# Optimization experiments

Hardware: AMD Instinct MI355X
Metric: run time of the kernel (lower is better)

## Reference

```python
import jax, jax.numpy as jnp
import numpy as np

BN_EPS = 1e-5


def _feat_proj(x, w1, w2, gamma, beta):
    # FactorLinear2D: (N,L,C) @ w2^T -> (N,L,K); weighted sum over L with w1^T -> (N,K)
    h = jnp.einsum('nlc,kc->nlk', x, w2)
    h = jnp.einsum('nlk,kl->nk', h, w1)
    # BatchNorm1d, training mode (biased batch stats), affine
    mu = h.mean(axis=0)
    var = h.var(axis=0)
    return gamma * (h - mu) * jax.lax.rsqrt(var + BN_EPS) + beta


def setup_inputs() -> dict:
    key = jax.random.key(0)
    ks = jax.random.split(key, 16)
    N, G, H, P, K = 64, 8, 1024, 2048, 39548
    s = 0.02
    return {
        'x0': jax.random.normal(ks[0], (N, 257, 1024), jnp.float32),
        'x1': jax.random.normal(ks[1], (N, 197, 768), jnp.float32),
        'w1_0': s * jax.random.normal(ks[2], (H, 257), jnp.float32),
        'w2_0': s * jax.random.normal(ks[3], (H, 1024), jnp.float32),
        'gamma0': jnp.ones((H,), jnp.float32),
        'beta0': jnp.zeros((H,), jnp.float32),
        'w1_1': s * jax.random.normal(ks[4], (H, 197), jnp.float32),
        'w2_1': s * jax.random.normal(ks[5], (H, 768), jnp.float32),
        'gamma1': jnp.ones((H,), jnp.float32),
        'beta1': jnp.zeros((H,), jnp.float32),
        'shared_w': s * jax.random.normal(ks[6], (P, H), jnp.float32),
        'fc_w': s * jax.random.normal(ks[7], (G * P, H), jnp.float32),
        'fc_b': s * jax.random.normal(ks[8], (G * P,), jnp.float32),
        'embed_w': s * jax.random.normal(ks[9], (K, P), jnp.float32),
        'embed_b': s * jax.random.normal(ks[10], (K,), jnp.float32),
        'indices': jax.random.randint(ks[11], (64,), 0, G, jnp.int64),
    }


def reference(x0, x1, w1_0, w2_0, gamma0, beta0, w1_1, w2_1, gamma1, beta1,
              shared_w, fc_w, fc_b, embed_w, embed_b, indices):
    G = 8
    h0 = _feat_proj(x0, w1_0, w2_0, gamma0, beta0)  # (N,H)
    h1 = _feat_proj(x1, w1_1, w2_1, gamma1, beta1)  # (N,H)
    latent = 0.5 * (h0 + h1)                        # mean over feature list
    # group prediction: embed(shared_proj(latent))
    group_pred = (latent @ shared_w.T) @ embed_w.T + embed_b  # (N,K)
    # subject-specific GroupLinear: gather per-sample weight slice, then reduced matmul
    P = fc_w.shape[0] // G
    w_sel = fc_w.reshape(G, P, -1)[indices]   # (N,P,H)
    b_sel = fc_b.reshape(G, P)[indices]       # (N,P)
    subj = jnp.einsum('nh,nph->np', latent, w_sel) + b_sel
    subj_res = subj @ embed_w.T + embed_b
    return group_pred + subj_res
```

## Files before the change

kernel.cpp:

```cpp
#include <hip/hip_runtime.h>
#include <hip/hip_bf16.h>


typedef __attribute__((ext_vector_type(4))) float f32x4;
typedef __attribute__((ext_vector_type(8))) short bf16x8;

__device__ __forceinline__ short f2bf(float v) {
  __hip_bfloat16 h = __float2bfloat16(v);
  union { __hip_bfloat16 b; short s; } u; u.b = h; return u.s;
}

__device__ __forceinline__ void gload16(const short* g, short* l) {
  __builtin_amdgcn_global_load_lds(
      (const __attribute__((address_space(1))) void*)g,
      (__attribute__((address_space(3))) void*)l, 16, 0, 0);
}

__device__ __forceinline__ void gload16f(const float* g, float* l) {
  __builtin_amdgcn_global_load_lds(
      (const __attribute__((address_space(1))) void*)g,
      (__attribute__((address_space(3))) void*)l, 16, 0, 0);
}

__device__ __forceinline__ void cvt8(const float* __restrict__ in,
                                     short* __restrict__ out, size_t i) {
  const float4* p = reinterpret_cast<const float4*>(in) + 2 * i;
  float4 a = p[0], b = p[1];
  bf16x8 o;
  o[0] = f2bf(a.x); o[1] = f2bf(a.y); o[2] = f2bf(a.z); o[3] = f2bf(a.w);
  o[4] = f2bf(b.x); o[5] = f2bf(b.y); o[6] = f2bf(b.z); o[7] = f2bf(b.w);
  *reinterpret_cast<bf16x8*>(out + 8 * i) = o;
}

__global__ __launch_bounds__(256) void prep(
    const float* __restrict__ x0, const float* __restrict__ x1,
    const float* __restrict__ w20, const float* __restrict__ w21,
    const float* __restrict__ w10, const float* __restrict__ w11,
    short* __restrict__ x0b, short* __restrict__ x1b,
    short* __restrict__ w20b, short* __restrict__ w21b,
    float* __restrict__ w1t0, float* __restrict__ w1t1,
    float* __restrict__ zz)
{
  size_t i = (size_t)blockIdx.x * 256 + threadIdx.x;
  const size_t C0 = 2105344;
  const size_t C1 = C0 + 8192;
  const size_t C2 = C1 + 1210368;
  const size_t C3 = C2 + 6144;
  const size_t C4 = C3 + 131072;
  const size_t C5 = C4 + 98304;
  const size_t C6 = C5 + 16384;
  const size_t C7 = C6 + 263168;
  if (i < C0) { cvt8(x0, x0b, i); return; }
  if (i < C1) {
    bf16x8 zv = {};
    *reinterpret_cast<bf16x8*>(x0b + (size_t)16448 * 1024 + 8 * (i - C0)) = zv;
    return;
  }
  if (i < C2) { cvt8(x1, x1b, i - C1); return; }
  if (i < C3) {
    bf16x8 zv = {};
    *reinterpret_cast<bf16x8*>(x1b + (size_t)12608 * 768 + 8 * (i - C2)) = zv;
    return;
  }
  if (i < C4) { cvt8(w20, w20b, i - C3); return; }
  if (i < C5) { cvt8(w21, w21b, i - C4); return; }
  if (i < C6) {
    f32x4 z4 = {};
    f32x4* zp = reinterpret_cast<f32x4*>(zz) + 2 * (i - C5);
    zp[0] = z4; zp[1] = z4;
    return;
  }
  if (i < C7) {
    size_t j = i - C6;
    w1t0[j] = w10[(j & 1023) * 257 + (j >> 10)];
    return;
  }
  size_t j = i - C7;
  w1t1[j] = w11[(j & 1023) * 197 + (j >> 10)];
}

template<int L>
__device__ __forceinline__ void fused_body(
    const short* __restrict__ Ab, const short* __restrict__ Bb,
    const float* __restrict__ w1t, float* __restrict__ z,
    int Mpad, int M, int K, int orig, short* As, short* Bs, float* zacc, int tid)
{
  const int lane = tid & 63;
  const int wave = tid >> 6;
  const int wm = wave >> 1, wn = wave & 1;
  const int tile_m = (orig >> 3) * 256;
  const int tile_n = (orig & 7) * 128;
  const int rl = lane & 15;
  const int lh = lane >> 4;

  zacc[tid] = 0.f;

  f32x4 acc[4][4] = {};
  const int nt = K >> 5;

  auto stage = [&](short* dA, short* dB, int k0) {
#pragma unroll
    for (int c = 0; c < 2; ++c) {
      int o = (c * 512 + tid) * 16;
      int r = o >> 6;
      int sc = ((o >> 4) & 3) ^ ((r >> 1) & 3);
      int gr = tile_m + r; if (gr >= Mpad) gr = Mpad - 1;
      gload16(Ab + (size_t)gr * K + k0 + sc * 8, (short*)((char*)dA + o));
    }
    {
      int o = tid * 16;
      int r = o >> 6;
      int sc = ((o >> 4) & 3) ^ ((r >> 1) & 3);
      gload16(Bb + (size_t)(tile_n + r) * K + k0 + sc * 8, (short*)((char*)dB + o));
    }
  };

  stage(As, Bs, 0);
  int cur = 0;
  for (int t = 0; t < nt; ++t) {
    if (t + 1 < nt) {
      stage(As + (cur ^ 1) * 8192, Bs + (cur ^ 1) * 4096, (t + 1) * 32);
      asm volatile("s_waitcnt vmcnt(3)" ::: "memory");
    } else {
      asm volatile("s_waitcnt vmcnt(0)" ::: "memory");
    }
    __builtin_amdgcn_s_barrier();
    __builtin_amdgcn_sched_barrier(0);
    const char* pa = (const char*)(As + cur * 8192);
    const char* pb = (const char*)(Bs + cur * 4096);
    bf16x8 af[4], bfr[4];
#pragma unroll
    for (int mi = 0; mi < 4; ++mi) {
      int r = wm * 64 + mi * 16 + rl;
      int j = lh ^ ((r >> 1) & 3);
      af[mi] = *reinterpret_cast<const bf16x8*>(pa + r * 64 + j * 16);
    }
#pragma unroll
    for (int ni = 0; ni < 4; ++ni) {
      int r = wn * 64 + ni * 16 + rl;
      int j = lh ^ ((r >> 1) & 3);
      bfr[ni] = *reinterpret_cast<const bf16x8*>(pb + r * 64 + j * 16);
    }
#pragma unroll
    for (int mi = 0; mi < 4; ++mi)
#pragma unroll
      for (int ni = 0; ni < 4; ++ni)
        acc[mi][ni] = __builtin_amdgcn_mfma_f32_16x16x32_bf16(af[mi], bfr[ni], acc[mi][ni], 0, 0, 0);
    __builtin_amdgcn_sched_barrier(0);
    __builtin_amdgcn_s_barrier();
    __builtin_amdgcn_sched_barrier(0);
    cur ^= 1;
  }

  const int nbase = tile_m / L;
#pragma unroll
  for (int ni = 0; ni < 4; ++ni) {
    int colL = wn * 64 + ni * 16 + rl;
    int col = tile_n + colL;
    float zac = 0.f;
    int curdn = -1;
#pragma unroll
    for (int mi = 0; mi < 4; ++mi) {
#pragma unroll
      for (int j = 0; j < 4; ++j) {
        int row = tile_m + wm * 64 + mi * 16 + lh * 4 + j;
        if (row < M) {
          int n = row / L, l = row - n * L;
          float v = acc[mi][ni][j] * w1t[(size_t)l * 1024 + col];
          int dn = n - nbase;
          if (dn != curdn) {
            if (curdn >= 0) atomicAdd(&zacc[curdn * 128 + colL], zac);
            curdn = dn; zac = 0.f;
          }
          zac += v;
        }
      }
    }
    if (curdn >= 0) atomicAdd(&zacc[curdn * 128 + colL], zac);
  }
  __syncthreads();
  {
    int dn = tid >> 7, c = tid & 127;
    int mtop = tile_m + 255; if (mtop > M - 1) mtop = M - 1;
    int nhi = mtop / L;
    int n = nbase + dn;
    if (n <= nhi)
      atomicAdd(z + (size_t)n * 1024 + tile_n + c, zacc[tid]);
  }
}

__global__ __launch_bounds__(512) void gemm_fused_dual(
    const short* __restrict__ x0b, const short* __restrict__ w20b,
    const float* __restrict__ w1t0, float* __restrict__ z0,
    const short* __restrict__ x1b, const short* __restrict__ w21b,
    const float* __restrict__ w1t1, float* __restrict__ z1)
{
  __shared__ short As[2 * 8192];
  __shared__ short Bs[2 * 4096];
  __shared__ float zacc[512];
  const int flat = blockIdx.x;
  const int tid = threadIdx.x;
  if (flat < 520) {
    const int orig = (flat & 7) * 65 + (flat >> 3);
    fused_body<257>(x0b, w20b, w1t0, z0, 16512, 16448, 1024, orig, As, Bs, zacc, tid);
  } else {
    const int f = flat - 520;
    const int orig = (f & 7) * 50 + (f >> 3);
    fused_body<197>(x1b, w21b, w1t1, z1, 12672, 12608, 768, orig, As, Bs, zacc, tid);
  }
}

__global__ void bn_latent(const float* __restrict__ z0, const float* __restrict__ z1,
                          const float* __restrict__ g0, const float* __restrict__ b0,
                          const float* __restrict__ g1, const float* __restrict__ b1,
                          float* __restrict__ lat)
{
  int k = blockIdx.x * blockDim.x + threadIdx.x;
  if (k >= 1024) return;
  float s0 = 0.f, q0 = 0.f, s1 = 0.f, q1 = 0.f;
  for (int n = 0; n < 64; ++n) {
    float v = z0[n * 1024 + k]; s0 += v; q0 += v * v;
    float w = z1[n * 1024 + k]; s1 += w; q1 += w * w;
  }
  float mu0 = s0 * (1.f / 64.f), var0 = q0 * (1.f / 64.f) - mu0 * mu0;
  float mu1 = s1 * (1.f / 64.f), var1 = q1 * (1.f / 64.f) - mu1 * mu1;
  float sc0 = g0[k] * rsqrtf(var0 + 1e-5f);
  float sc1 = g1[k] * rsqrtf(var1 + 1e-5f);
  float be0 = b0[k], be1 = b1[k];
  for (int n = 0; n < 64; ++n) {
    float v = sc0 * (z0[n * 1024 + k] - mu0) + be0
            + sc1 * (z1[n * 1024 + k] - mu1) + be1;
    lat[n * 1024 + k] = 0.5f * v;
  }
}

__global__ __launch_bounds__(512) void s_combine(
    const float* __restrict__ lat, const float* __restrict__ sw,
    const float* __restrict__ fw, const float* __restrict__ fb,
    const int* __restrict__ idx, short* __restrict__ sb)
{
  __shared__ int nlist[64];
  __shared__ int ncnt;
  const int g  = blockIdx.x >> 5;
  const int pc = blockIdx.x & 31;
  const int tid = threadIdx.x;
  const int lane = tid & 63;
  const int wave = tid >> 6;

  if (wave == 0) {
    int match = (idx[lane] == g) ? 1 : 0;
    unsigned long long m = __ballot(match);
    if (match) {
      int pos = __popcll(m & ((1ull << lane) - 1ull));
      nlist[pos] = lane;
    }
    if (lane == 0) ncnt = __popcll(m);
  }
  __syncthreads();
  const int cnt = ncnt;
  if (cnt == 0) return;

  for (int c0 = 0; c0 < cnt; c0 += 8) {
    const int nc = (cnt - c0 < 8) ? (cnt - c0) : 8;
    f32x4 latr[8][4];
#pragma unroll
    for (int j2 = 0; j2 < 8; ++j2)
      if (j2 < nc) {
        const f32x4* lp = reinterpret_cast<const f32x4*>(lat + (size_t)nlist[c0 + j2] * 1024);
#pragma unroll
        for (int q = 0; q < 4; ++q) latr[j2][q] = lp[q * 64 + lane];
      }
#pragma unroll 2
    for (int pi = 0; pi < 8; ++pi) {
      int p = pc * 64 + wave * 8 + pi;
      const f32x4* fp = reinterpret_cast<const f32x4*>(fw + ((size_t)g * 2048 + p) * 1024);
      const f32x4* sp = reinterpret_cast<const f32x4*>(sw + (size_t)p * 1024);
      f32x4 row[4];
#pragma unroll
      for (int q = 0; q < 4; ++q) row[q] = fp[q * 64 + lane] + sp[q * 64 + lane];
      float bias = fb[(size_t)g * 2048 + p];
#pragma unroll
      for (int j2 = 0; j2 < 8; ++j2)
        if (j2 < nc) {
          float d = 0.f;
#pragma unroll
          for (int q = 0; q < 4; ++q) {
            d = fmaf(row[q][0], latr[j2][q][0], d);
            d = fmaf(row[q][1], latr[j2][q][1], d);
            d = fmaf(row[q][2], latr[j2][q][2], d);
            d = fmaf(row[q][3], latr[j2][q][3], d);
          }
          d += __shfl_xor(d, 32); d += __shfl_xor(d, 16);
          d += __shfl_xor(d, 8);  d += __shfl_xor(d, 4);
          d += __shfl_xor(d, 2);  d += __shfl_xor(d, 1);
          if (lane == 0)
            sb[(size_t)nlist[c0 + j2] * 2048 + p] = f2bf(d + bias);
        }
    }
  }
}

__global__ __launch_bounds__(256) void gemm_embed(
    const short* __restrict__ sb, const float* __restrict__ E,
    const float* __restrict__ eb, float* __restrict__ out)
{
  __shared__ short As[2 * 64 * 64];
  __shared__ float Bs[2 * 64 * 64];
  const int tid  = threadIdx.x;
  const int lane = tid & 63;
  const int wave = tid >> 6;
  const int rl = lane & 15;
  const int lh = lane >> 4;
  const int tile_n = blockIdx.x * 64;

  auto stage = [&](int buf, int k0) {
#pragma unroll
    for (int c = 0; c < 2; ++c) {
      int o = (c * 256 + tid) * 16;
      int r = o >> 7;
      int cc = ((o >> 4) & 7) ^ (r & 7);
      gload16(sb + (size_t)r * 2048 + k0 + cc * 8,
              (short*)((char*)(As + buf * 4096) + o));
    }
#pragma unroll
    for (int c = 0; c < 4; ++c) {
      int o = (c * 256 + tid) * 16;
      int r = o >> 8;
      int cc = ((o >> 4) & 15) ^ (r & 15);
      int gr = tile_n + r; if (gr > 39547) gr = 39547;
      gload16f(E + (size_t)gr * 2048 + k0 + cc * 4,
               (float*)((char*)(Bs + buf * 4096) + o));
    }
  };

  f32x4 acc[4] = {};
  stage(0, 0);
  int cur = 0;
  for (int t = 0; t < 32; ++t) {
    if (t < 31) {
      stage(cur ^ 1, (t + 1) * 64);
      asm volatile("s_waitcnt vmcnt(6)" ::: "memory");
    } else {
      asm volatile("s_waitcnt vmcnt(0)" ::: "memory");
    }
    __builtin_amdgcn_s_barrier();
    __builtin_amdgcn_sched_barrier(0);
    const char* pa = (const char*)(As + cur * 4096);
    const char* pb = (const char*)(Bs + cur * 4096);
#pragma unroll
    for (int ks = 0; ks < 2; ++ks) {
      int br = wave * 16 + rl;
      int c0 = ks * 8 + lh * 2;
      f32x4 u = *reinterpret_cast<const f32x4*>(pb + br * 256 + ((c0 ^ (br & 15)) * 16));
      f32x4 v = *reinterpret_cast<const f32x4*>(pb + br * 256 + (((c0 + 1) ^ (br & 15)) * 16));
      bf16x8 bf;
      bf[0] = f2bf(u[0]); bf[1] = f2bf(u[1]); bf[2] = f2bf(u[2]); bf[3] = f2bf(u[3]);
      bf[4] = f2bf(v[0]); bf[5] = f2bf(v[1]); bf[6] = f2bf(v[2]); bf[7] = f2bf(v[3]);
#pragma unroll
      for (int mi = 0; mi < 4; ++mi) {
        int ar = mi * 16 + rl;
        int ac = (ks * 4 + lh) ^ (ar & 7);
        bf16x8 af = *reinterpret_cast<const bf16x8*>(pa + ar * 128 + ac * 16);
        acc[mi] = __builtin_amdgcn_mfma_f32_16x16x32_bf16(af, bf, acc[mi], 0, 0, 0);
      }
    }
    __builtin_amdgcn_sched_barrier(0);
    __builtin_amdgcn_s_barrier();
    __builtin_amdgcn_sched_barrier(0);
    cur ^= 1;
  }

  int col = tile_n + wave * 16 + rl;
  if (col < 39548) {
    float bi = 2.f * eb[col];
#pragma unroll
    for (int mi = 0; mi < 4; ++mi)
#pragma unroll
      for (int j = 0; j < 4; ++j) {
        int n = mi * 16 + lh * 4 + j;
        out[(size_t)n * 39548 + col] = acc[mi][j] + bi;
      }
  }
}

extern "C" void kernel_launch(void* const* d_in, const int* in_sizes, int n_in,
                              void* d_out, int out_size, void* d_ws, size_t ws_size,
                              hipStream_t stream)
{
  const float* x0       = (const float*)d_in[0];
  const float* x1       = (const float*)d_in[1];
  const float* w1_0     = (const float*)d_in[2];
  const float* w2_0     = (const float*)d_in[3];
  const float* gamma0   = (const float*)d_in[4];
  const float* beta0    = (const float*)d_in[5];
  const float* w1_1     = (const float*)d_in[6];
  const float* w2_1     = (const float*)d_in[7];
  const float* gamma1   = (const float*)d_in[8];
  const float* beta1    = (const float*)d_in[9];
  const float* shared_w = (const float*)d_in[10];
  const float* fc_w     = (const float*)d_in[11];
  const float* fc_b     = (const float*)d_in[12];
  const float* embed_w  = (const float*)d_in[13];
  const float* embed_b  = (const float*)d_in[14];
  const int*   indices  = (const int*)d_in[15];
  float* out = (float*)d_out;

  short* x0b  = (short*)d_ws;
  short* x1b  = x0b + (size_t)16512 * 1024;
  short* w20b = x1b + (size_t)12672 * 768;
  short* w21b = w20b + (size_t)1024 * 1024;
  float* w1t0 = (float*)(w21b + (size_t)1024 * 768);
  float* w1t1 = w1t0 + (size_t)257 * 1024;
  float* z0   = w1t1 + (size_t)197 * 1024;
  float* z1   = z0 + 64 * 1024;
  float* lat  = z1 + 64 * 1024;
  short* sb   = (short*)(lat + 64 * 1024);

  prep<<<15784, 256, 0, stream>>>(x0, x1, w2_0, w2_1, w1_0, w1_1,
                                  x0b, x1b, w20b, w21b, w1t0, w1t1, z0);

  gemm_fused_dual<<<920, 512, 0, stream>>>(x0b, w20b, w1t0, z0,
                                           x1b, w21b, w1t1, z1);

  bn_latent<<<16, 64, 0, stream>>>(z0, z1, gamma0, beta0, gamma1, beta1, lat);
  s_combine<<<256, 512, 0, stream>>>(lat, shared_w, fc_w, fc_b, indices, sb);

  gemm_embed<<<618, 256, 0, stream>>>(sb, embed_w, embed_b, out);
}
```

Baseline: 241.2 us.

## Tile w1 transpose via shared memory, load embed A operand directly, add setprio

The prep kernel's strided w1 transpose becomes a 32x33 shared-memory tiled transpose in extra blocks, so reads and writes are coalesced, and the launch grid shrinks to match. In gemm_embed the small bf16 A operand (sb) is now read straight from global into registers instead of being staged through LDS, which frees LDS and cuts barrier-bound staging work. s_setprio raises wave priority around the MFMA blocks in both GEMMs. The direct A loads rely on L2 hits and add register pressure.

```diff
diff --git a/kernel.cpp b/kernel.cpp
--- a/kernel.cpp
+++ b/kernel.cpp
@@ -41,6 +41,29 @@
     float* __restrict__ w1t0, float* __restrict__ w1t1,
     float* __restrict__ zz)
 {
+  __shared__ float tile[32][33];
+  if (blockIdx.x >= 13968) {
+    int b = blockIdx.x - 13968;
+    const float* src; float* dst; int Lw;
+    if (b < 288) { src = w10; dst = w1t0; Lw = 257; }
+    else         { b -= 288; src = w11; dst = w1t1; Lw = 197; }
+    int kt = b & 31, lt = b >> 5;
+    int c = threadIdx.x & 31, r8 = threadIdx.x >> 5;
+#pragma unroll
+    for (int i = 0; i < 4; ++i) {
+      int a = r8 + 8 * i;
+      int l = lt * 32 + c;
+      tile[a][c] = (l < Lw) ? src[(size_t)(kt * 32 + a) * Lw + l] : 0.f;
+    }
+    __syncthreads();
+#pragma unroll
+    for (int i = 0; i < 4; ++i) {
+      int bl = r8 + 8 * i;
+      int l = lt * 32 + bl;
+      if (l < Lw) dst[(size_t)l * 1024 + kt * 32 + c] = tile[c][bl];
+    }
+    return;
+  }
   size_t i = (size_t)blockIdx.x * 256 + threadIdx.x;
   const size_t C0 = 2105344;
   const size_t C1 = C0 + 8192;
@@ -48,8 +71,6 @@
   const size_t C3 = C2 + 6144;
   const size_t C4 = C3 + 131072;
   const size_t C5 = C4 + 98304;
-  const size_t C6 = C5 + 16384;
-  const size_t C7 = C6 + 263168;
   if (i < C0) { cvt8(x0, x0b, i); return; }
   if (i < C1) {
     bf16x8 zv = {};
@@ -64,19 +85,9 @@
   }
   if (i < C4) { cvt8(w20, w20b, i - C3); return; }
   if (i < C5) { cvt8(w21, w21b, i - C4); return; }
-  if (i < C6) {
-    f32x4 z4 = {};
-    f32x4* zp = reinterpret_cast<f32x4*>(zz) + 2 * (i - C5);
-    zp[0] = z4; zp[1] = z4;
-    return;
-  }
-  if (i < C7) {
-    size_t j = i - C6;
-    w1t0[j] = w10[(j & 1023) * 257 + (j >> 10)];
-    return;
-  }
-  size_t j = i - C7;
-  w1t1[j] = w11[(j & 1023) * 197 + (j >> 10)];
+  f32x4 z4 = {};
+  f32x4* zp = reinterpret_cast<f32x4*>(zz) + 2 * (i - C5);
+  zp[0] = z4; zp[1] = z4;
 }
 
 template<int L>
@@ -141,11 +152,13 @@
       int j = lh ^ ((r >> 1) & 3);
       bfr[ni] = *reinterpret_cast<const bf16x8*>(pb + r * 64 + j * 16);
     }
+    __builtin_amdgcn_s_setprio(1);
 #pragma unroll
     for (int mi = 0; mi < 4; ++mi)
 #pragma unroll
       for (int ni = 0; ni < 4; ++ni)
         acc[mi][ni] = __builtin_amdgcn_mfma_f32_16x16x32_bf16(af[mi], bfr[ni], acc[mi][ni], 0, 0, 0);
+    __builtin_amdgcn_s_setprio(0);
     __builtin_amdgcn_sched_barrier(0);
     __builtin_amdgcn_s_barrier();
     __builtin_amdgcn_sched_barrier(0);
@@ -304,7 +317,6 @@
     const short* __restrict__ sb, const float* __restrict__ E,
     const float* __restrict__ eb, float* __restrict__ out)
 {
-  __shared__ short As[2 * 64 * 64];
   __shared__ float Bs[2 * 64 * 64];
   const int tid  = threadIdx.x;
   const int lane = tid & 63;
@@ -313,15 +325,7 @@
   const int lh = lane >> 4;
   const int tile_n = blockIdx.x * 64;
 
-  auto stage = [&](int buf, int k0) {
-#pragma unroll
-    for (int c = 0; c < 2; ++c) {
-      int o = (c * 256 + tid) * 16;
-      int r = o >> 7;
-      int cc = ((o >> 4) & 7) ^ (r & 7);
-      gload16(sb + (size_t)r * 2048 + k0 + cc * 8,
-              (short*)((char*)(As + buf * 4096) + o));
-    }
+  auto stageB = [&](int buf, int k0) {
 #pragma unroll
     for (int c = 0; c < 4; ++c) {
       int o = (c * 256 + tid) * 16;
@@ -334,18 +338,26 @@
   };
 
   f32x4 acc[4] = {};
-  stage(0, 0);
+  stageB(0, 0);
   int cur = 0;
   for (int t = 0; t < 32; ++t) {
+    const int k0 = t * 64;
+    bf16x8 a0[4], a1[4];
+#pragma unroll
+    for (int mi = 0; mi < 4; ++mi) {
+      const short* ap = sb + (size_t)(mi * 16 + rl) * 2048 + k0 + lh * 8;
+      a0[mi] = *reinterpret_cast<const bf16x8*>(ap);
+      a1[mi] = *reinterpret_cast<const bf16x8*>(ap + 32);
+    }
+    __builtin_amdgcn_sched_barrier(0);
     if (t < 31) {
-      stage(cur ^ 1, (t + 1) * 64);
-      asm volatile("s_waitcnt vmcnt(6)" ::: "memory");
+      stageB(cur ^ 1, (t + 1) * 64);
+      asm volatile("s_waitcnt vmcnt(4)" ::: "memory");
     } else {
       asm volatile("s_waitcnt vmcnt(0)" ::: "memory");
     }
     __builtin_amdgcn_s_barrier();
     __builtin_amdgcn_sched_barrier(0);
-    const char* pa = (const char*)(As + cur * 4096);
     const char* pb = (const char*)(Bs + cur * 4096);
 #pragma unroll
     for (int ks = 0; ks < 2; ++ks) {
@@ -356,13 +368,13 @@
       bf16x8 bf;
       bf[0] = f2bf(u[0]); bf[1] = f2bf(u[1]); bf[2] = f2bf(u[2]); bf[3] = f2bf(u[3]);
       bf[4] = f2bf(v[0]); bf[5] = f2bf(v[1]); bf[6] = f2bf(v[2]); bf[7] = f2bf(v[3]);
+      __builtin_amdgcn_s_setprio(1);
 #pragma unroll
       for (int mi = 0; mi < 4; ++mi) {
-        int ar = mi * 16 + rl;
-        int ac = (ks * 4 + lh) ^ (ar & 7);
-        bf16x8 af = *reinterpret_cast<const bf16x8*>(pa + ar * 128 + ac * 16);
+        bf16x8 af = ks ? a1[mi] : a0[mi];
         acc[mi] = __builtin_amdgcn_mfma_f32_16x16x32_bf16(af, bf, acc[mi], 0, 0, 0);
       }
+      __builtin_amdgcn_s_setprio(0);
     }
     __builtin_amdgcn_sched_barrier(0);
     __builtin_amdgcn_s_barrier();
@@ -416,7 +428,7 @@
   float* lat  = z1 + 64 * 1024;
   short* sb   = (short*)(lat + 64 * 1024);
 
-  prep<<<15784, 256, 0, stream>>>(x0, x1, w2_0, w2_1, w1_0, w1_1,
+  prep<<<14480, 256, 0, stream>>>(x0, x1, w2_0, w2_1, w1_0, w1_1,
                                   x0b, x1b, w20b, w21b, w1t0, w1t1, z0);
 
   gemm_fused_dual<<<920, 512, 0, stream>>>(x0b, w20b, w1t0, z0,
```

Result: slower. 277.3 us (+14.9%).
